# Optimization experiments

Hardware: AMD Instinct MI355X
Metric: run time of the kernel (lower is better)

The kernel has to match this reference:

```python
import jax, jax.numpy as jnp
import numpy as np

B, S = 1, 2048
HIDDEN = 2560
NH, NKV, HD = 32, 8, 128
GS = 128  # awq group size
ROPE_THETA = 1000000.0


def dequant_q4(qweight, scales, qzeros):
    """Unpack int4 AWQ weights -> dense [K, N] float weight.
    qweight: [K//8, N] int32, 8 nibbles packed along the input (K) dim.
    scales/qzeros: [K//GS, N]. w = (nibble - zero) * scale.
    """
    K8, N = qweight.shape
    shifts = jnp.arange(8, dtype=jnp.int32) * 4
    nib = (qweight[:, None, :] >> shifts[None, :, None]) & 0xF  # [K//8, 8, N]
    w = nib.reshape(K8 * 8, N).astype(scales.dtype)             # [K, N]
    z = jnp.repeat(qzeros.astype(scales.dtype), GS, axis=0)     # [K, N]
    s = jnp.repeat(scales, GS, axis=0)                          # [K, N]
    return (w - z) * s


def linear_q4(x, qw, sc, qz, bias=None):
    w = dequant_q4(qw, sc, qz)                     # [K, N]
    y = jnp.einsum('bsk,kn->bsn', x, w)
    return y + bias if bias is not None else y


def rotate_half(x):
    x1, x2 = jnp.split(x, 2, axis=-1)
    return jnp.concatenate([-x2, x1], axis=-1)


def apply_rope(q, k, cos, sin):
    # cos/sin: [B, S, HD] -> broadcast over heads at dim 2
    c = cos[:, :, None, :]
    s = sin[:, :, None, :]
    return q * c + rotate_half(q) * s, k * c + rotate_half(k) * s


def setup_inputs() -> dict:
    key = jax.random.key(0)
    ks = jax.random.split(key, 12)

    x = jax.random.normal(ks[0], (B, S, HIDDEN), dtype=jnp.float32)

    # genuine rotary embedding tables
    inv_freq = 1.0 / (ROPE_THETA ** (np.arange(0, HD, 2, dtype=np.float32) / HD))
    t = np.arange(S, dtype=np.float32)
    freqs = np.outer(t, inv_freq)                      # [S, HD/2]
    emb = np.concatenate([freqs, freqs], axis=-1)      # [S, HD]
    cos = jnp.asarray(np.cos(emb)[None], dtype=jnp.float32)  # [1, S, HD]
    sin = jnp.asarray(np.sin(emb)[None], dtype=jnp.float32)

    def mk_proj(kq, ksc, kz, K, N, group=GS):
        qw = jax.random.randint(kq, (K // 8, N), 0, 2**31 - 1, dtype=jnp.int32)
        sc = jax.random.normal(ksc, (K // group, N), dtype=jnp.float32) * 0.01
        qz = jax.random.randint(kz, (K // group, N), 0, 16, dtype=jnp.int32)
        return qw, sc, qz

    q_qweight, q_scales, q_qzeros = mk_proj(ks[1], ks[2], ks[3], HIDDEN, NH * HD)
    k_qweight, k_scales, k_qzeros = mk_proj(ks[4], ks[5], ks[6], HIDDEN, NKV * HD)
    v_qweight, v_scales, v_qzeros = mk_proj(ks[7], ks[8], ks[9], HIDDEN, NKV * HD)
    o_qweight, o_scales, o_qzeros = mk_proj(ks[10], ks[11], jax.random.fold_in(key, 99), NH * HD, HIDDEN)

    kb = jax.random.split(jax.random.fold_in(key, 7), 3)
    q_bias = jax.random.normal(kb[0], (NH * HD,), dtype=jnp.float32) * 0.02
    k_bias = jax.random.normal(kb[1], (NKV * HD,), dtype=jnp.float32) * 0.02
    v_bias = jax.random.normal(kb[2], (NKV * HD,), dtype=jnp.float32) * 0.02

    return dict(x=x, cos=cos, sin=sin,
                q_scales=q_scales, q_bias=q_bias,
                k_scales=k_scales, k_bias=k_bias,
                v_scales=v_scales, v_bias=v_bias,
                o_scales=o_scales,
                q_qweight=q_qweight, q_qzeros=q_qzeros,
                k_qweight=k_qweight, k_qzeros=k_qzeros,
                v_qweight=v_qweight, v_qzeros=v_qzeros,
                o_qweight=o_qweight, o_qzeros=o_qzeros)


def reference(x, cos, sin,
              q_scales, q_bias, k_scales, k_bias, v_scales, v_bias, o_scales,
              q_qweight, q_qzeros, k_qweight, k_qzeros,
              v_qweight, v_qzeros, o_qweight, o_qzeros):
    b, s, _ = x.shape
    xq = linear_q4(x, q_qweight, q_scales, q_qzeros, q_bias).reshape(b, s, NH, HD)
    xk = linear_q4(x, k_qweight, k_scales, k_qzeros, k_bias).reshape(b, s, NKV, HD)
    xv = linear_q4(x, v_qweight, v_scales, v_qzeros, v_bias).reshape(b, s, NKV, HD)

    xq, xk = apply_rope(xq, xk, cos, sin)

    # GQA: repeat KV heads to match query heads (prefill, start_pos=0)
    rep = NH // NKV
    xk = jnp.repeat(xk, rep, axis=2)   # [b, s, NH, HD]
    xv = jnp.repeat(xv, rep, axis=2)

    scale = 1.0 / jnp.sqrt(jnp.asarray(HD, dtype=xq.dtype))
    scores = jnp.einsum('bqhd,bkhd->bhqk', xq, xk) * scale  # [b, NH, s, s]
    causal = jnp.tril(jnp.ones((s, s), dtype=bool))
    scores = jnp.where(causal[None, None], scores, jnp.finfo(scores.dtype).min)
    attn = jax.nn.softmax(scores, axis=-1)
    out = jnp.einsum('bhqk,bkhd->bqhd', attn, xv).reshape(b, s, NH * HD)

    return linear_q4(out, o_qweight, o_scales, o_qzeros)  # [b, s, HIDDEN]
```

## Files before the change

### kernel.cpp

```cpp
#include <hip/hip_runtime.h>
#include <hip/hip_bf16.h>
#include <cstdint>

#define S_LEN 2048
#define HIDDEN 2560
#define NH 32
#define NKV 8
#define HD 128
#define GS 128

typedef __attribute__((ext_vector_type(8))) _Float16 half8v;
typedef __attribute__((ext_vector_type(2))) _Float16 half2v;
typedef __attribute__((ext_vector_type(4))) float f32x4;
typedef unsigned int uint;
typedef unsigned short ushort;

__device__ inline ushort f2h(float f) {
    _Float16 h = (_Float16)f;
    return __builtin_bit_cast(ushort, h);
}
__device__ inline float h2f(ushort u) {
    return (float)__builtin_bit_cast(_Float16, u);
}
__device__ inline uint pk2(ushort a, ushort b) { return (uint)a | ((uint)b << 16); }

__device__ __attribute__((always_inline)) inline void gl_lds16(const void* g, void* l) {
    __builtin_amdgcn_global_load_lds(
        (const __attribute__((address_space(1))) unsigned int*)g,
        (__attribute__((address_space(3))) unsigned int*)l, 16, 0, 0);
}

#define WAIT_LGKM0  asm volatile("s_waitcnt lgkmcnt(0)" ::: "memory")
#define WAIT_VM(N)  asm volatile("s_waitcnt vmcnt(" #N ")" ::: "memory")
#define RAW_BARRIER { __builtin_amdgcn_s_barrier(); __builtin_amdgcn_sched_barrier(0); }

__global__ __launch_bounds__(320) void xcvt_kernel(
    const float* __restrict__ X, ushort* __restrict__ Xf)
{
    const int row = blockIdx.x;
    const int t   = threadIdx.x;
    const size_t base = (size_t)row * HIDDEN + t * 8;
    float4 a = *(const float4*)&X[base];
    float4 b = *(const float4*)&X[base + 4];
    uint4 hw = {pk2(f2h(a.x), f2h(a.y)), pk2(f2h(a.z), f2h(a.w)),
                pk2(f2h(b.x), f2h(b.y)), pk2(f2h(b.z), f2h(b.w))};
    *(uint4*)&Xf[base] = hw;
}

__global__ __launch_bounds__(256) void qkv9_kernel(
    const ushort* __restrict__ Xf,
    const int* __restrict__ q_qw, const float* __restrict__ q_sc,
    const int* __restrict__ q_qz, const float* __restrict__ q_b,
    const int* __restrict__ k_qw, const float* __restrict__ k_sc,
    const int* __restrict__ k_qz, const float* __restrict__ k_b,
    const int* __restrict__ v_qw, const float* __restrict__ v_sc,
    const int* __restrict__ v_qz, const float* __restrict__ v_b,
    const float* __restrict__ cosb, const float* __restrict__ sinb,
    ushort* __restrict__ Qf, ushort* __restrict__ Kf,
    ushort* __restrict__ Vrm)
{
    __shared__ __align__(16) char LDSB[65536];
    ushort* A0 = (ushort*)(LDSB);
    ushort* A1 = (ushort*)(LDSB + 16384);
    ushort* B0 = (ushort*)(LDSB + 32768);
    ushort* B1 = (ushort*)(LDSB + 49152);

    const int t  = threadIdx.x;
    const int w  = t >> 6;
    const int l  = t & 63;
    const int lg = l >> 4;
    const int lr = l & 15;
    const int wr = w >> 1;
    const int wc = w & 1;
    const int K  = HIDDEN;

    const int bid = blockIdx.x;
    const int swz = (bid & 7) * 96 + (bid >> 3);
    const int nblk = swz % 48;
    const int m0   = (swz / 48) * 128;

    int region, nbase, Nw;
    const int* QW; const float* SC; const int* QZ; const float* BI;
    if (nblk < 32)      { region = 0; nbase = nblk * 128;        Nw = NH * HD;
                          QW = q_qw; SC = q_sc; QZ = q_qz; BI = q_b; }
    else if (nblk < 40) { region = 1; nbase = (nblk - 32) * 128; Nw = NKV * HD;
                          QW = k_qw; SC = k_sc; QZ = k_qz; BI = k_b; }
    else                { region = 2; nbase = (nblk - 40) * 128; Nw = NKV * HD;
                          QW = v_qw; SC = v_sc; QZ = v_qz; BI = v_b; }

    const int ldsAw = w * 1024;
    size_t aoff[4];
#pragma unroll
    for (int i = 0; i < 4; ++i) {
        int slot = i * 256 + t;
        int am = slot >> 3, ac = slot & 7;
        aoff[i] = (size_t)(m0 + am) * K + (size_t)((ac ^ (am & 7)) * 8);
    }
    const int bn  = t & 127;
    const int bk0 = (t >> 7) * 4;
    int bwoff[4];
#pragma unroll
    for (int j = 0; j < 4; ++j)
        bwoff[j] = (bn * 128 + (bk0 + j) * 16) ^ ((bn & 7) << 4);

    int ncm[4];
#pragma unroll
    for (int nf = 0; nf < 4; ++nf)
        ncm[nf] = wc * 32 + (nf & 1) * 16 + lr + ((nf & 2) ? 64 : 0);

    const int xorA = (lr & 7) << 4;
    int aroff[4][2], broff[4][2];
#pragma unroll
    for (int mf = 0; mf < 4; ++mf)
#pragma unroll
        for (int ks = 0; ks < 2; ++ks)
            aroff[mf][ks] = (((wr * 64 + mf * 16 + lr) * 128) + lg * 16 + ks * 64) ^ xorA;
#pragma unroll
    for (int nf = 0; nf < 4; ++nf)
#pragma unroll
        for (int ks = 0; ks < 2; ++ks)
            broff[nf][ks] = ((ncm[nf] * 128) + lg * 16 + ks * 64) ^ xorA;

    f32x4 macc[4][4];
#pragma unroll
    for (int mf = 0; mf < 4; ++mf)
#pragma unroll
        for (int nf = 0; nf < 4; ++nf) macc[mf][nf] = f32x4{0.f, 0.f, 0.f, 0.f};
    uint qr[4];
    float scf, zf;

#define QKV_QW(tile) { int g8 = (tile) * 8; int gg = (tile) >> 1; \
    _Pragma("unroll") \
    for (int j = 0; j < 4; ++j) \
        qr[j] = (uint)QW[(size_t)(g8 + bk0 + j) * Nw + nbase + bn]; \
    scf = SC[(size_t)gg * Nw + nbase + bn]; \
    zf  = (float)QZ[(size_t)gg * Nw + nbase + bn]; }

#define QKV_STAGE_A(AH, k0) { \
    gl_lds16(Xf + (k0) + aoff[0], (char*)(AH) + ldsAw); \
    gl_lds16(Xf + (k0) + aoff[1], (char*)(AH) + 4096 + ldsAw); \
    gl_lds16(Xf + (k0) + aoff[2], (char*)(AH) + 8192 + ldsAw); \
    gl_lds16(Xf + (k0) + aoff[3], (char*)(AH) + 12288 + ldsAw); }

#define QKV_BWRITE(BT) { \
    ushort sch = f2h(scf); \
    float schf = h2f(sch); \
    ushort msc = f2h(-128.0f * schf);    \
    ushort nzs = f2h(-(zf * schf)); \
    half2v S2 = {__builtin_bit_cast(_Float16, sch), __builtin_bit_cast(_Float16, sch)}; \
    half2v M2 = {__builtin_bit_cast(_Float16, msc), __builtin_bit_cast(_Float16, msc)}; \
    half2v Z2 = {__builtin_bit_cast(_Float16, nzs), __builtin_bit_cast(_Float16, nzs)}; \
    _Pragma("unroll") \
    for (int j = 0; j < 4; ++j) { \
        uint q = qr[j]; \
        uint xn = q & 0x0F0F0F0Fu; \
        uint yn = (q >> 4) & 0x0F0F0F0Fu; \
        uint4 dw; \
        uint W0 = __builtin_amdgcn_perm(yn, xn, 0x0C040C00u); \
        uint W1 = __builtin_amdgcn_perm(yn, xn, 0x0C050C01u); \
        uint W2 = __builtin_amdgcn_perm(yn, xn, 0x0C060C02u); \
        uint W3 = __builtin_amdgcn_perm(yn, xn, 0x0C070C03u); \
        uint e0 = (W0 << 3) | 0x58005800u; \
        uint e1 = (W1 << 3) | 0x58005800u; \
        uint e2 = (W2 << 3) | 0x58005800u; \
        uint e3 = (W3 << 3) | 0x58005800u; \
        half2v w0 = __builtin_bit_cast(half2v, e0) * S2 + M2; w0 = w0 + Z2; \
        half2v w1 = __builtin_bit_cast(half2v, e1) * S2 + M2; w1 = w1 + Z2; \
        half2v w2 = __builtin_bit_cast(half2v, e2) * S2 + M2; w2 = w2 + Z2; \
        half2v w3 = __builtin_bit_cast(half2v, e3) * S2 + M2; w3 = w3 + Z2; \
        dw.x = __builtin_bit_cast(uint, w0); \
        dw.y = __builtin_bit_cast(uint, w1); \
        dw.z = __builtin_bit_cast(uint, w2); \
        dw.w = __builtin_bit_cast(uint, w3); \
        *(uint4*)((char*)(BT) + bwoff[j]) = dw; \
    } }

#define QKV_COMPUTE(AH, BT) { \
    _Pragma("unroll") \
    for (int ks = 0; ks < 2; ++ks) { \
        half8v av[4], bv[4]; \
        _Pragma("unroll") \
        for (int mf = 0; mf < 4; ++mf) \
            av[mf] = *(const half8v*)((const char*)(AH) + aroff[mf][ks]); \
        _Pragma("unroll") \
        for (int nf = 0; nf < 4; ++nf) \
            bv[nf] = *(const half8v*)((const char*)(BT) + broff[nf][ks]); \
        _Pragma("unroll") \
        for (int mf = 0; mf < 4; ++mf) \
            _Pragma("unroll") \
            for (int nf = 0; nf < 4; ++nf) \
                macc[mf][nf] = __builtin_amdgcn_mfma_f32_16x16x32_f16(av[mf], bv[nf], macc[mf][nf], 0, 0, 0); \
    } }

    QKV_QW(0);
    QKV_BWRITE(B0);
    QKV_STAGE_A(A0, 0);
    QKV_QW(1);
    WAIT_LGKM0;
    WAIT_VM(6);
    RAW_BARRIER;

    for (int g = 0; g < 19; ++g) {
        QKV_STAGE_A(A1, (2 * g + 1) * 64);
        QKV_COMPUTE(A0, B0);
        QKV_BWRITE(B1);
        QKV_QW(2 * g + 2);
        WAIT_LGKM0;
        WAIT_VM(6);
        RAW_BARRIER;
        QKV_STAGE_A(A0, (2 * g + 2) * 64);
        QKV_COMPUTE(A1, B1);
        QKV_BWRITE(B0);
        QKV_QW(2 * g + 3);
        WAIT_LGKM0;
        WAIT_VM(6);
        RAW_BARRIER;
    }
    QKV_STAGE_A(A1, 39 * 64);
    QKV_COMPUTE(A0, B0);
    QKV_BWRITE(B1);
    WAIT_LGKM0;
    WAIT_VM(0);
    RAW_BARRIER;
    QKV_COMPUTE(A1, B1);

#pragma unroll
    for (int nf = 0; nf < 4; ++nf) {
        float bv = BI[nbase + ncm[nf]];
#pragma unroll
        for (int mf = 0; mf < 4; ++mf)
#pragma unroll
            for (int r = 0; r < 4; ++r) macc[mf][nf][r] += bv;
    }

    if (region == 2) {
#pragma unroll
        for (int mf = 0; mf < 4; ++mf)
#pragma unroll
            for (int r = 0; r < 4; ++r) {
                int row = m0 + wr * 64 + mf * 16 + lg * 4 + r;
#pragma unroll
                for (int nf = 0; nf < 4; ++nf)
                    Vrm[(size_t)row * (NKV * HD) + nbase + ncm[nf]] = f2h(macc[mf][nf][r]);
            }
    } else {
        ushort* OF = (region == 0) ? Qf : Kf;
        const int No = (region == 0) ? NH * HD : NKV * HD;
        const float osc = (region == 0) ? 0.08838834764831845f : 1.0f;
#pragma unroll
        for (int mf = 0; mf < 4; ++mf)
#pragma unroll
            for (int r = 0; r < 4; ++r) {
                int row = m0 + wr * 64 + mf * 16 + lg * 4 + r;
                const float* cb = &cosb[(size_t)row * HD];
                const float* sb = &sinb[(size_t)row * HD];
#pragma unroll
                for (int nf = 0; nf < 2; ++nf) {
                    int d = wc * 32 + nf * 16 + lr;
                    float a = macc[mf][nf][r];
                    float b = macc[mf][nf + 2][r];
                    float o1 = (a * cb[d]      - b * sb[d])      * osc;
                    float o2 = (b * cb[d + 64] + a * sb[d + 64]) * osc;
                    OF[(size_t)row * No + nbase + d]      = f2h(o1);
                    OF[(size_t)row * No + nbase + d + 64] = f2h(o2);
                }
            }
    }
#undef QKV_QW
#undef QKV_STAGE_A
#undef QKV_BWRITE
#undef QKV_COMPUTE
}

__global__ __launch_bounds__(256) void vtrans_kernel(
    const ushort* __restrict__ Vrm, ushort* __restrict__ VfT)
{
    __shared__ ushort Ts[64][65];
    const int s0 = blockIdx.x * 64;
    const int n0 = blockIdx.y * 64;
    const int t  = threadIdx.x;
    {
        int r = t >> 2, c0 = (t & 3) * 16;
        uint4 v0 = *(const uint4*)&Vrm[(size_t)(s0 + r) * (NKV * HD) + n0 + c0];
        uint4 v1 = *(const uint4*)&Vrm[(size_t)(s0 + r) * (NKV * HD) + n0 + c0 + 8];
        const ushort* pv = (const ushort*)&v0;
#pragma unroll
        for (int j = 0; j < 8; ++j) Ts[r][c0 + j] = pv[j];
        pv = (const ushort*)&v1;
#pragma unroll
        for (int j = 0; j < 8; ++j) Ts[r][c0 + 8 + j] = pv[j];
    }
    __syncthreads();
    {
        int rn = t >> 2, cs0 = (t & 3) * 16;
        ushort ob[16];
#pragma unroll
        for (int j = 0; j < 16; ++j) ob[j] = Ts[cs0 + j][rn];
        ushort* dst = &VfT[(size_t)(n0 + rn) * S_LEN + s0 + cs0];
        *(uint4*)dst = ((uint4*)ob)[0];
        *(uint4*)(dst + 8) = ((uint4*)ob)[1];
    }
}

__global__ __launch_bounds__(256) void oproj8_kernel(
    const ushort* __restrict__ Xb, const int* __restrict__ QW,
    const float* __restrict__ SC, const int* __restrict__ QZ,
    float* __restrict__ Y)
{
    __shared__ __align__(16) char LDSB[65536];
    ushort* A0 = (ushort*)(LDSB);
    ushort* A1 = (ushort*)(LDSB + 16384);
    ushort* B0 = (ushort*)(LDSB + 32768);
    ushort* B1 = (ushort*)(LDSB + 49152);

    const int t  = threadIdx.x;
    const int w  = t >> 6;
    const int l  = t & 63;
    const int lg = l >> 4;
    const int lr = l & 15;
    const int wr = w >> 1;
    const int wc = w & 1;
    const int K  = NH * HD;
    const int N  = HIDDEN;

    const int bid = blockIdx.x;
    const int swz = (bid & 7) * 40 + (bid >> 3);
    const int n0  = (swz % 20) * 128;
    const int m0  = (swz / 20) * 128;

    const int ldsAw = w * 1024;
    size_t aoff[4];
#pragma unroll
    for (int i = 0; i < 4; ++i) {
        int slot = i * 256 + t;
        int am = slot >> 3, ac = slot & 7;
        aoff[i] = (size_t)(m0 + am) * K + (size_t)((ac ^ (am & 7)) * 8);
    }
    const int bn  = t & 127;
    const int bk0 = (t >> 7) * 4;
    int bwoff[4];
#pragma unroll
    for (int j = 0; j < 4; ++j)
        bwoff[j] = (bn * 128 + (bk0 + j) * 16) ^ ((bn & 7) << 4);

    const int xorA = (lr & 7) << 4;
    int aroff[4][2], broff[4][2];
#pragma unroll
    for (int mf = 0; mf < 4; ++mf)
#pragma unroll
        for (int ks = 0; ks < 2; ++ks)
            aroff[mf][ks] = (((wr * 64 + mf * 16 + lr) * 128) + lg * 16 + ks * 64) ^ xorA;
#pragma unroll
    for (int nf = 0; nf < 4; ++nf)
#pragma unroll
        for (int ks = 0; ks < 2; ++ks)
            broff[nf][ks] = (((wc * 64 + nf * 16 + lr) * 128) + lg * 16 + ks * 64) ^ xorA;

    f32x4 macc[4][4];
#pragma unroll
    for (int mf = 0; mf < 4; ++mf)
#pragma unroll
        for (int nf = 0; nf < 4; ++nf) macc[mf][nf] = f32x4{0.f, 0.f, 0.f, 0.f};
    uint qr[4];
    float scf, zf;

#define OP_QW(tile) { int g8 = (tile) * 8; int gg = (tile) >> 1; \
    _Pragma("unroll") \
    for (int j = 0; j < 4; ++j) \
        qr[j] = (uint)QW[(size_t)(g8 + bk0 + j) * N + n0 + bn]; \
    scf = SC[(size_t)gg * N + n0 + bn]; \
    zf  = (float)QZ[(size_t)gg * N + n0 + bn]; }

#define OP_STAGE_A(AH, k0) { \
    gl_lds16(Xb + (k0) + aoff[0], (char*)(AH) + ldsAw); \
    gl_lds16(Xb + (k0) + aoff[1], (char*)(AH) + 4096 + ldsAw); \
    gl_lds16(Xb + (k0) + aoff[2], (char*)(AH) + 8192 + ldsAw); \
    gl_lds16(Xb + (k0) + aoff[3], (char*)(AH) + 12288 + ldsAw); }

#define OP_BWRITE(BT) { \
    ushort sch = f2h(scf); \
    float schf = h2f(sch); \
    ushort msc = f2h(-128.0f * schf); \
    ushort nzs = f2h(-(zf * schf)); \
    half2v S2 = {__builtin_bit_cast(_Float16, sch), __builtin_bit_cast(_Float16, sch)}; \
    half2v M2 = {__builtin_bit_cast(_Float16, msc), __builtin_bit_cast(_Float16, msc)}; \
    half2v Z2 = {__builtin_bit_cast(_Float16, nzs), __builtin_bit_cast(_Float16, nzs)}; \
    _Pragma("unroll") \
    for (int j = 0; j < 4; ++j) { \
        uint q = qr[j]; \
        uint xn = q & 0x0F0F0F0Fu; \
        uint yn = (q >> 4) & 0x0F0F0F0Fu; \
        uint4 dw; \
        uint W0 = __builtin_amdgcn_perm(yn, xn, 0x0C040C00u); \
        uint W1 = __builtin_amdgcn_perm(yn, xn, 0x0C050C01u); \
        uint W2 = __builtin_amdgcn_perm(yn, xn, 0x0C060C02u); \
        uint W3 = __builtin_amdgcn_perm(yn, xn, 0x0C070C03u); \
        uint e0 = (W0 << 3) | 0x58005800u; \
        uint e1 = (W1 << 3) | 0x58005800u; \
        uint e2 = (W2 << 3) | 0x58005800u; \
        uint e3 = (W3 << 3) | 0x58005800u; \
        half2v w0 = __builtin_bit_cast(half2v, e0) * S2 + M2; w0 = w0 + Z2; \
        half2v w1 = __builtin_bit_cast(half2v, e1) * S2 + M2; w1 = w1 + Z2; \
        half2v w2 = __builtin_bit_cast(half2v, e2) * S2 + M2; w2 = w2 + Z2; \
        half2v w3 = __builtin_bit_cast(half2v, e3) * S2 + M2; w3 = w3 + Z2; \
        dw.x = __builtin_bit_cast(uint, w0); \
        dw.y = __builtin_bit_cast(uint, w1); \
        dw.z = __builtin_bit_cast(uint, w2); \
        dw.w = __builtin_bit_cast(uint, w3); \
        *(uint4*)((char*)(BT) + bwoff[j]) = dw; \
    } }

#define OP_COMPUTE(AH, BT) { \
    _Pragma("unroll") \
    for (int ks = 0; ks < 2; ++ks) { \
        half8v av[4], bv[4]; \
        _Pragma("unroll") \
        for (int mf = 0; mf < 4; ++mf) \
            av[mf] = *(const half8v*)((const char*)(AH) + aroff[mf][ks]); \
        _Pragma("unroll") \
        for (int nf = 0; nf < 4; ++nf) \
            bv[nf] = *(const half8v*)((const char*)(BT) + broff[nf][ks]); \
        _Pragma("unroll") \
        for (int mf = 0; mf < 4; ++mf) \
            _Pragma("unroll") \
            for (int nf = 0; nf < 4; ++nf) \
                macc[mf][nf] = __builtin_amdgcn_mfma_f32_16x16x32_f16(av[mf], bv[nf], macc[mf][nf], 0, 0, 0); \
    } }

    OP_QW(0);
    OP_BWRITE(B0);
    OP_STAGE_A(A0, 0);
    OP_QW(1);
    WAIT_LGKM0;
    WAIT_VM(6);
    RAW_BARRIER;

    for (int g = 0; g < 31; ++g) {
        OP_STAGE_A(A1, (2 * g + 1) * 64);
        OP_COMPUTE(A0, B0);
        OP_BWRITE(B1);
        OP_QW(2 * g + 2);
        WAIT_LGKM0;
        WAIT_VM(6);
        RAW_BARRIER;
        OP_STAGE_A(A0, (2 * g + 2) * 64);
        OP_COMPUTE(A1, B1);
        OP_BWRITE(B0);
        OP_QW(2 * g + 3);
        WAIT_LGKM0;
        WAIT_VM(6);
        RAW_BARRIER;
    }
    OP_STAGE_A(A1, 63 * 64);
    OP_COMPUTE(A0, B0);
    OP_BWRITE(B1);
    WAIT_LGKM0;
    WAIT_VM(0);
    RAW_BARRIER;
    OP_COMPUTE(A1, B1);

#pragma unroll
    for (int mf = 0; mf < 4; ++mf)
#pragma unroll
        for (int r = 0; r < 4; ++r) {
            int row = m0 + wr * 64 + mf * 16 + lg * 4 + r;
#pragma unroll
            for (int nf = 0; nf < 4; ++nf)
                Y[(size_t)row * N + n0 + wc * 64 + nf * 16 + lr] = macc[mf][nf][r];
        }
#undef OP_QW
#undef OP_STAGE_A
#undef OP_BWRITE
#undef OP_COMPUTE
}

__global__ __launch_bounds__(256) void attn_mfma_kernel(
    const ushort* __restrict__ Qh,
    const ushort* __restrict__ Kh,
    const ushort* __restrict__ Vt,
    ushort* __restrict__ AO)
{
    __shared__ ushort Ks0[32 * 128];
    __shared__ ushort Ks1[32 * 128];
    __shared__ ushort Vs0[128 * 32];
    __shared__ ushort Vs1[128 * 32];
    __shared__ __align__(16) char PsB[4 * 1280];

    const int h  = blockIdx.x;
    const int qb = gridDim.y - 1 - blockIdx.y;
    const int s0 = qb * 64;
    const int t  = threadIdx.x;
    const int w  = t >> 6;
    const int l  = t & 63;
    const int lg = l >> 4;
    const int lr = l & 15;
    const int kvh = h >> 2;
    const int qw = s0 + w * 16;
    const int q  = qw + lr;

    half8v qf[4];
#pragma unroll
    for (int d = 0; d < 4; ++d) {
        size_t off = (size_t)q * (NH * HD) + h * HD + d * 32 + lg * 8;
        qf[d] = *(const half8v*)&Qh[off];
    }

    f32x4 o[8];
#pragma unroll
    for (int i = 0; i < 8; ++i) o[i] = f32x4{0.f, 0.f, 0.f, 0.f};
    float m = -1e30f, lsum = 0.f;
    char* pw = PsB + w * 1280;

#define ATTN_STAGE(KB, VB, k0) { \
    _Pragma("unroll") \
    for (int i = 0; i < 2; ++i) { \
        int slot = w * 128 + i * 64 + l; \
        int mr = slot >> 4, c = slot & 15; \
        size_t goff = (size_t)((k0) + mr) * (NKV * HD) + kvh * HD + ((c ^ (mr & 7)) * 8); \
        gl_lds16(Kh + goff, (char*)(KB) + (w * 128 + i * 64) * 16); \
    } \
    _Pragma("unroll") \
    for (int i = 0; i < 2; ++i) { \
        int slot = w * 128 + i * 64 + l; \
        int dim = slot >> 2, c = slot & 3; \
        size_t goff = (size_t)(kvh * HD + dim) * S_LEN + (k0) + ((c ^ (dim & 3)) * 8); \
        gl_lds16(Vt + goff, (char*)(VB) + (w * 128 + i * 64) * 16); \
    } }

#define ATTN_TILE(KSF, VSS, k0) \
    if ((k0) <= qw + 15) { \
        f32x4 s_[2]; \
        s_[0] = f32x4{0.f, 0.f, 0.f, 0.f}; \
        s_[1] = f32x4{0.f, 0.f, 0.f, 0.f}; \
        _Pragma("unroll") \
        for (int d = 0; d < 4; ++d) { \
            _Pragma("unroll") \
            for (int nt2 = 0; nt2 < 2; ++nt2) { \
                int row = nt2 * 16 + lr; \
                int off = row * 256 + ((d * 64 + lg * 16) ^ ((row & 7) << 4)); \
                half8v kf = *(const half8v*)((const char*)(KSF) + off); \
                s_[nt2] = __builtin_amdgcn_mfma_f32_16x16x32_f16(kf, qf[d], s_[nt2], 0, 0, 0); \
            } \
        } \
        float sv[8]; \
        _Pragma("unroll") \
        for (int nt2 = 0; nt2 < 2; ++nt2) \
            _Pragma("unroll") \
            for (int r = 0; r < 4; ++r) { \
                int kv = (k0) + nt2 * 16 + lg * 4 + r; \
                sv[nt2 * 4 + r] = (kv <= q) ? s_[nt2][r] : -1e30f; \
            } \
        float mx = sv[0]; \
        _Pragma("unroll") \
        for (int j = 1; j < 8; ++j) mx = fmaxf(mx, sv[j]); \
        mx = fmaxf(mx, __shfl_xor(mx, 16)); \
        mx = fmaxf(mx, __shfl_xor(mx, 32)); \
        float mnew = fmaxf(m, mx); \
        float resc = __expf(m - mnew); \
        m = mnew; \
        float p_[8], ps = 0.f; \
        _Pragma("unroll") \
        for (int j = 0; j < 8; ++j) { p_[j] = __expf(sv[j] - mnew); ps += p_[j]; } \
        ps += __shfl_xor(ps, 16); \
        ps += __shfl_xor(ps, 32); \
        lsum = lsum * resc + ps; \
        _Pragma("unroll") \
        for (int dt = 0; dt < 8; ++dt) \
            _Pragma("unroll") \
            for (int r = 0; r < 4; ++r) o[dt][r] *= resc; \
        uint2 w0_ = {pk2(f2h(p_[0]), f2h(p_[1])), pk2(f2h(p_[2]), f2h(p_[3]))}; \
        uint2 w1_ = {pk2(f2h(p_[4]), f2h(p_[5])), pk2(f2h(p_[6]), f2h(p_[7]))}; \
        *(uint2*)(pw + lr * 80 + lg * 8)      = w0_; \
        *(uint2*)(pw + lr * 80 + 32 + lg * 8) = w1_; \
        asm volatile("s_waitcnt lgkmcnt(0)" ::: "memory"); \
        half8v pf = *(const half8v*)(pw + lr * 80 + lg * 16); \
        _Pragma("unroll") \
        for (int dt = 0; dt < 8; ++dt) { \
            int dim = dt * 16 + lr; \
            half8v vf = *(const half8v*)((const char*)(VSS) + dim * 64 + ((lg * 16) ^ ((dim & 3) << 4))); \
            o[dt] = __builtin_amdgcn_mfma_f32_16x16x32_f16(vf, pf, o[dt], 0, 0, 0); \
        } \
    }

    const int ntiles = qb * 2 + 2;

    ATTN_STAGE(Ks0, Vs0, 0);
    WAIT_VM(0);
    RAW_BARRIER;

    for (int kt = 0; kt < ntiles; kt += 2) {
        if (kt + 1 < ntiles) ATTN_STAGE(Ks1, Vs1, (kt + 1) * 32);
        ATTN_TILE(Ks0, Vs0, kt * 32);
        WAIT_VM(0);
        RAW_BARRIER;
        if (kt + 2 < ntiles) ATTN_STAGE(Ks0, Vs0, (kt + 2) * 32);
        ATTN_TILE(Ks1, Vs1, (kt + 1) * 32);
        WAIT_VM(0);
        RAW_BARRIER;
    }

    float inv = 1.f / lsum;
    ushort* dst = &AO[(size_t)q * (NH * HD) + h * HD];
#pragma unroll
    for (int dt = 0; dt < 8; ++dt) {
        uint2 ov = {pk2(f2h(o[dt][0] * inv), f2h(o[dt][1] * inv)),
                    pk2(f2h(o[dt][2] * inv), f2h(o[dt][3] * inv))};
        *(uint2*)(dst + dt * 16 + lg * 4) = ov;
    }
#undef ATTN_STAGE
#undef ATTN_TILE
}

extern "C" void kernel_launch(void* const* d_in, const int* in_sizes, int n_in,
                              void* d_out, int out_size, void* d_ws, size_t ws_size,
                              hipStream_t stream)
{
    const float* x    = (const float*)d_in[0];
    const float* cosb = (const float*)d_in[1];
    const float* sinb = (const float*)d_in[2];
    const float* q_sc = (const float*)d_in[3];
    const float* q_b  = (const float*)d_in[4];
    const float* k_sc = (const float*)d_in[5];
    const float* k_b  = (const float*)d_in[6];
    const float* v_sc = (const float*)d_in[7];
    const float* v_b  = (const float*)d_in[8];
    const float* o_sc = (const float*)d_in[9];
    const int* q_qw   = (const int*)d_in[10];
    const int* q_qz   = (const int*)d_in[11];
    const int* k_qw   = (const int*)d_in[12];
    const int* k_qz   = (const int*)d_in[13];
    const int* v_qw   = (const int*)d_in[14];
    const int* v_qz   = (const int*)d_in[15];
    const int* o_qw   = (const int*)d_in[16];
    const int* o_qz   = (const int*)d_in[17];
    float* out = (float*)d_out;

    char* ws = (char*)d_ws;
    ushort* Xf   = (ushort*)ws;
    ushort* AOf  = (ushort*)ws;
    ushort* Qf   = (ushort*)(ws + (size_t)16 * 1024 * 1024);
    ushort* Kf   = (ushort*)(ws + (size_t)32 * 1024 * 1024);
    ushort* Vrm  = (ushort*)(ws + (size_t)36 * 1024 * 1024);
    ushort* VfT  = (ushort*)(ws + (size_t)40 * 1024 * 1024);

    xcvt_kernel<<<S_LEN, 320, 0, stream>>>(x, Xf);

    qkv9_kernel<<<768, 256, 0, stream>>>(
        Xf,
        q_qw, q_sc, q_qz, q_b,
        k_qw, k_sc, k_qz, k_b,
        v_qw, v_sc, v_qz, v_b,
        cosb, sinb, Qf, Kf, Vrm);

    vtrans_kernel<<<dim3(S_LEN / 64, (NKV * HD) / 64), 256, 0, stream>>>(Vrm, VfT);

    attn_mfma_kernel<<<dim3(NH, S_LEN / 64), 256, 0, stream>>>(Qf, Kf, VfT, AOf);

    oproj8_kernel<<<320, 256, 0, stream>>>(
        AOf, o_qw, o_sc, o_qz, out);
}
```

Measured before the change: 259.9 us.

## Split QKV weight dequant into separate pre-pass kernel feeding plain fp16 GEMM

Moves the int4 AWQ dequantization out of the QKV GEMM main loop into a dedicated kernel that writes a transposed fp16 weight matrix WT to workspace once. The GEMM then streams both X and WT tiles via direct global-to-LDS loads, with no in-loop unpacking. Each 128-column weight tile was previously dequantized once for every one of the 16 row-blocks, so this removes that redundant ALU work. The cost is an extra launch and roughly 15 MB of fp16 weight traffic. The wait is now vmcnt(0) each stage, which weakens prefetch overlap.

```diff
diff --git a/kernel.cpp b/kernel.cpp
--- a/kernel.cpp
+++ b/kernel.cpp
@@ -47,14 +47,75 @@
     *(uint4*)&Xf[base] = hw;
 }
 
-__global__ __launch_bounds__(256) void qkv9_kernel(
-    const ushort* __restrict__ Xf,
-    const int* __restrict__ q_qw, const float* __restrict__ q_sc,
-    const int* __restrict__ q_qz, const float* __restrict__ q_b,
-    const int* __restrict__ k_qw, const float* __restrict__ k_sc,
-    const int* __restrict__ k_qz, const float* __restrict__ k_b,
-    const int* __restrict__ v_qw, const float* __restrict__ v_sc,
-    const int* __restrict__ v_qz, const float* __restrict__ v_b,
+__global__ __launch_bounds__(256) void wdq_kernel(
+    const int* __restrict__ q_qw, const float* __restrict__ q_sc, const int* __restrict__ q_qz,
+    const int* __restrict__ k_qw, const float* __restrict__ k_sc, const int* __restrict__ k_qz,
+    const int* __restrict__ v_qw, const float* __restrict__ v_sc, const int* __restrict__ v_qz,
+    ushort* __restrict__ WT)
+{
+    __shared__ __align__(16) char Ts[16384];
+
+    const int bx = blockIdx.x;
+    const int kt = blockIdx.y;
+    const int t  = threadIdx.x;
+
+    int nloc0, wtbase, Nw;
+    const int* QW; const float* SC; const int* QZ;
+    if (bx < 64)      { Nw = NH * HD;  nloc0 = bx * 64;        wtbase = bx * 64;
+                        QW = q_qw; SC = q_sc; QZ = q_qz; }
+    else if (bx < 80) { Nw = NKV * HD; nloc0 = (bx - 64) * 64; wtbase = 4096 + nloc0;
+                        QW = k_qw; SC = k_sc; QZ = k_qz; }
+    else              { Nw = NKV * HD; nloc0 = (bx - 80) * 64; wtbase = 5120 + nloc0;
+                        QW = v_qw; SC = v_sc; QZ = v_qz; }
+
+    const int k80 = kt * 16;
+    const int nn  = t & 63;
+    const float scf = SC[(size_t)kt * Nw + nloc0 + nn];
+    const float zf  = (float)QZ[(size_t)kt * Nw + nloc0 + nn];
+    ushort sch = f2h(scf);
+    float schf = h2f(sch);
+    ushort msc = f2h(-128.0f * schf);
+    ushort nzs = f2h(-(zf * schf));
+    half2v S2 = {__builtin_bit_cast(_Float16, sch), __builtin_bit_cast(_Float16, sch)};
+    half2v M2 = {__builtin_bit_cast(_Float16, msc), __builtin_bit_cast(_Float16, msc)};
+    half2v Z2 = {__builtin_bit_cast(_Float16, nzs), __builtin_bit_cast(_Float16, nzs)};
+
+#pragma unroll
+    for (int i = 0; i < 4; ++i) {
+        int kw = i * 4 + (t >> 6);
+        uint q = (uint)QW[(size_t)(k80 + kw) * Nw + nloc0 + nn];
+        uint xn = q & 0x0F0F0F0Fu;
+        uint yn = (q >> 4) & 0x0F0F0F0Fu;
+        uint W0 = __builtin_amdgcn_perm(yn, xn, 0x0C040C00u);
+        uint W1 = __builtin_amdgcn_perm(yn, xn, 0x0C050C01u);
+        uint W2 = __builtin_amdgcn_perm(yn, xn, 0x0C060C02u);
+        uint W3 = __builtin_amdgcn_perm(yn, xn, 0x0C070C03u);
+        uint e0 = (W0 << 3) | 0x58005800u;
+        uint e1 = (W1 << 3) | 0x58005800u;
+        uint e2 = (W2 << 3) | 0x58005800u;
+        uint e3 = (W3 << 3) | 0x58005800u;
+        half2v w0 = __builtin_bit_cast(half2v, e0) * S2 + M2; w0 = w0 + Z2;
+        half2v w1 = __builtin_bit_cast(half2v, e1) * S2 + M2; w1 = w1 + Z2;
+        half2v w2 = __builtin_bit_cast(half2v, e2) * S2 + M2; w2 = w2 + Z2;
+        half2v w3 = __builtin_bit_cast(half2v, e3) * S2 + M2; w3 = w3 + Z2;
+        uint4 dw = {__builtin_bit_cast(uint, w0), __builtin_bit_cast(uint, w1),
+                    __builtin_bit_cast(uint, w2), __builtin_bit_cast(uint, w3)};
+        *(uint4*)(Ts + nn * 256 + ((kw * 16) ^ ((nn & 7) << 4))) = dw;
+    }
+    __syncthreads();
+    const int kc = t & 15;
+#pragma unroll
+    for (int i = 0; i < 4; ++i) {
+        int nr = i * 16 + (t >> 4);
+        uint4 v = *(const uint4*)(Ts + nr * 256 + ((kc * 16) ^ ((nr & 7) << 4)));
+        *(uint4*)&WT[(size_t)(wtbase + nr) * HIDDEN + kt * 128 + kc * 8] = v;
+    }
+}
+
+__global__ __launch_bounds__(256) void qkv10_kernel(
+    const ushort* __restrict__ Xf, const ushort* __restrict__ WT,
+    const float* __restrict__ q_b, const float* __restrict__ k_b,
+    const float* __restrict__ v_b,
     const float* __restrict__ cosb, const float* __restrict__ sinb,
     ushort* __restrict__ Qf, ushort* __restrict__ Kf,
     ushort* __restrict__ Vrm)
@@ -78,30 +139,23 @@
     const int swz = (bid & 7) * 96 + (bid >> 3);
     const int nblk = swz % 48;
     const int m0   = (swz / 48) * 128;
-
-    int region, nbase, Nw;
-    const int* QW; const float* SC; const int* QZ; const float* BI;
-    if (nblk < 32)      { region = 0; nbase = nblk * 128;        Nw = NH * HD;
-                          QW = q_qw; SC = q_sc; QZ = q_qz; BI = q_b; }
-    else if (nblk < 40) { region = 1; nbase = (nblk - 32) * 128; Nw = NKV * HD;
-                          QW = k_qw; SC = k_sc; QZ = k_qz; BI = k_b; }
-    else                { region = 2; nbase = (nblk - 40) * 128; Nw = NKV * HD;
-                          QW = v_qw; SC = v_sc; QZ = v_qz; BI = v_b; }
+    const int wtrow = nblk * 128;
+
+    int region, nbase;
+    const float* BI;
+    if (nblk < 32)      { region = 0; nbase = nblk * 128;        BI = q_b; }
+    else if (nblk < 40) { region = 1; nbase = (nblk - 32) * 128; BI = k_b; }
+    else                { region = 2; nbase = (nblk - 40) * 128; BI = v_b; }
 
     const int ldsAw = w * 1024;
-    size_t aoff[4];
+    size_t aoff[4], boff[4];
 #pragma unroll
     for (int i = 0; i < 4; ++i) {
         int slot = i * 256 + t;
-        int am = slot >> 3, ac = slot & 7;
-        aoff[i] = (size_t)(m0 + am) * K + (size_t)((ac ^ (am & 7)) * 8);
-    }
-    const int bn  = t & 127;
-    const int bk0 = (t >> 7) * 4;
-    int bwoff[4];
-#pragma unroll
-    for (int j = 0; j < 4; ++j)
-        bwoff[j] = (bn * 128 + (bk0 + j) * 16) ^ ((bn & 7) << 4);
+        int rm = slot >> 3, rc = slot & 7;
+        aoff[i] = (size_t)(m0 + rm) * K + (size_t)((rc ^ (rm & 7)) * 8);
+        boff[i] = (size_t)(wtrow + rm) * K + (size_t)((rc ^ (rm & 7)) * 8);
+    }
 
     int ncm[4];
 #pragma unroll
@@ -126,54 +180,16 @@
     for (int mf = 0; mf < 4; ++mf)
 #pragma unroll
         for (int nf = 0; nf < 4; ++nf) macc[mf][nf] = f32x4{0.f, 0.f, 0.f, 0.f};
-    uint qr[4];
-    float scf, zf;
-
-#define QKV_QW(tile) { int g8 = (tile) * 8; int gg = (tile) >> 1; \
-    _Pragma("unroll") \
-    for (int j = 0; j < 4; ++j) \
-        qr[j] = (uint)QW[(size_t)(g8 + bk0 + j) * Nw + nbase + bn]; \
-    scf = SC[(size_t)gg * Nw + nbase + bn]; \
-    zf  = (float)QZ[(size_t)gg * Nw + nbase + bn]; }
-
-#define QKV_STAGE_A(AH, k0) { \
+
+#define QKV_STAGE(AH, BH, k0) { \
     gl_lds16(Xf + (k0) + aoff[0], (char*)(AH) + ldsAw); \
     gl_lds16(Xf + (k0) + aoff[1], (char*)(AH) + 4096 + ldsAw); \
     gl_lds16(Xf + (k0) + aoff[2], (char*)(AH) + 8192 + ldsAw); \
-    gl_lds16(Xf + (k0) + aoff[3], (char*)(AH) + 12288 + ldsAw); }
-
-#define QKV_BWRITE(BT) { \
-    ushort sch = f2h(scf); \
-    float schf = h2f(sch); \
-    ushort msc = f2h(-128.0f * schf);    \
-    ushort nzs = f2h(-(zf * schf)); \
-    half2v S2 = {__builtin_bit_cast(_Float16, sch), __builtin_bit_cast(_Float16, sch)}; \
-    half2v M2 = {__builtin_bit_cast(_Float16, msc), __builtin_bit_cast(_Float16, msc)}; \
-    half2v Z2 = {__builtin_bit_cast(_Float16, nzs), __builtin_bit_cast(_Float16, nzs)}; \
-    _Pragma("unroll") \
-    for (int j = 0; j < 4; ++j) { \
-        uint q = qr[j]; \
-        uint xn = q & 0x0F0F0F0Fu; \
-        uint yn = (q >> 4) & 0x0F0F0F0Fu; \
-        uint4 dw; \
-        uint W0 = __builtin_amdgcn_perm(yn, xn, 0x0C040C00u); \
-        uint W1 = __builtin_amdgcn_perm(yn, xn, 0x0C050C01u); \
-        uint W2 = __builtin_amdgcn_perm(yn, xn, 0x0C060C02u); \
-        uint W3 = __builtin_amdgcn_perm(yn, xn, 0x0C070C03u); \
-        uint e0 = (W0 << 3) | 0x58005800u; \
-        uint e1 = (W1 << 3) | 0x58005800u; \
-        uint e2 = (W2 << 3) | 0x58005800u; \
-        uint e3 = (W3 << 3) | 0x58005800u; \
-        half2v w0 = __builtin_bit_cast(half2v, e0) * S2 + M2; w0 = w0 + Z2; \
-        half2v w1 = __builtin_bit_cast(half2v, e1) * S2 + M2; w1 = w1 + Z2; \
-        half2v w2 = __builtin_bit_cast(half2v, e2) * S2 + M2; w2 = w2 + Z2; \
-        half2v w3 = __builtin_bit_cast(half2v, e3) * S2 + M2; w3 = w3 + Z2; \
-        dw.x = __builtin_bit_cast(uint, w0); \
-        dw.y = __builtin_bit_cast(uint, w1); \
-        dw.z = __builtin_bit_cast(uint, w2); \
-        dw.w = __builtin_bit_cast(uint, w3); \
-        *(uint4*)((char*)(BT) + bwoff[j]) = dw; \
-    } }
+    gl_lds16(Xf + (k0) + aoff[3], (char*)(AH) + 12288 + ldsAw); \
+    gl_lds16(WT + (k0) + boff[0], (char*)(BH) + ldsAw); \
+    gl_lds16(WT + (k0) + boff[1], (char*)(BH) + 4096 + ldsAw); \
+    gl_lds16(WT + (k0) + boff[2], (char*)(BH) + 8192 + ldsAw); \
+    gl_lds16(WT + (k0) + boff[3], (char*)(BH) + 12288 + ldsAw); }
 
 #define QKV_COMPUTE(AH, BT) { \
     _Pragma("unroll") \
@@ -192,34 +208,22 @@
                 macc[mf][nf] = __builtin_amdgcn_mfma_f32_16x16x32_f16(av[mf], bv[nf], macc[mf][nf], 0, 0, 0); \
     } }
 
-    QKV_QW(0);
-    QKV_BWRITE(B0);
-    QKV_STAGE_A(A0, 0);
-    QKV_QW(1);
-    WAIT_LGKM0;
-    WAIT_VM(6);
+    QKV_STAGE(A0, B0, 0);
+    WAIT_VM(0);
     RAW_BARRIER;
 
     for (int g = 0; g < 19; ++g) {
-        QKV_STAGE_A(A1, (2 * g + 1) * 64);
+        QKV_STAGE(A1, B1, (2 * g + 1) * 64);
         QKV_COMPUTE(A0, B0);
-        QKV_BWRITE(B1);
-        QKV_QW(2 * g + 2);
-        WAIT_LGKM0;
-        WAIT_VM(6);
+        WAIT_VM(0);
         RAW_BARRIER;
-        QKV_STAGE_A(A0, (2 * g + 2) * 64);
+        QKV_STAGE(A0, B0, (2 * g + 2) * 64);
         QKV_COMPUTE(A1, B1);
-        QKV_BWRITE(B0);
-        QKV_QW(2 * g + 3);
-        WAIT_LGKM0;
-        WAIT_VM(6);
+        WAIT_VM(0);
         RAW_BARRIER;
     }
-    QKV_STAGE_A(A1, 39 * 64);
+    QKV_STAGE(A1, B1, 39 * 64);
     QKV_COMPUTE(A0, B0);
-    QKV_BWRITE(B1);
-    WAIT_LGKM0;
     WAIT_VM(0);
     RAW_BARRIER;
     QKV_COMPUTE(A1, B1);
@@ -266,9 +270,7 @@
                 }
             }
     }
-#undef QKV_QW
-#undef QKV_STAGE_A
-#undef QKV_BWRITE
+#undef QKV_STAGE
 #undef QKV_COMPUTE
 }
 
@@ -638,19 +640,19 @@
     char* ws = (char*)d_ws;
     ushort* Xf   = (ushort*)ws;
     ushort* AOf  = (ushort*)ws;
-    ushort* Qf   = (ushort*)(ws + (size_t)16 * 1024 * 1024);
-    ushort* Kf   = (ushort*)(ws + (size_t)32 * 1024 * 1024);
-    ushort* Vrm  = (ushort*)(ws + (size_t)36 * 1024 * 1024);
-    ushort* VfT  = (ushort*)(ws + (size_t)40 * 1024 * 1024);
+    ushort* WT   = (ushort*)(ws + (size_t)10 * 1024 * 1024);
+    ushort* Qf   = (ushort*)(ws + (size_t)40 * 1024 * 1024);
+    ushort* Kf   = (ushort*)(ws + (size_t)56 * 1024 * 1024);
+    ushort* Vrm  = (ushort*)(ws + (size_t)60 * 1024 * 1024);
+    ushort* VfT  = (ushort*)(ws + (size_t)64 * 1024 * 1024);
 
     xcvt_kernel<<<S_LEN, 320, 0, stream>>>(x, Xf);
 
-    qkv9_kernel<<<768, 256, 0, stream>>>(
-        Xf,
-        q_qw, q_sc, q_qz, q_b,
-        k_qw, k_sc, k_qz, k_b,
-        v_qw, v_sc, v_qz, v_b,
-        cosb, sinb, Qf, Kf, Vrm);
+    wdq_kernel<<<dim3(96, 20), 256, 0, stream>>>(
+        q_qw, q_sc, q_qz, k_qw, k_sc, k_qz, v_qw, v_sc, v_qz, WT);
+
+    qkv10_kernel<<<768, 256, 0, stream>>>(
+        Xf, WT, q_b, k_b, v_b, cosb, sinb, Qf, Kf, Vrm);
 
     vtrans_kernel<<<dim3(S_LEN / 64, (NKV * HD) / 64), 256, 0, stream>>>(Vrm, VfT);
 
```

After: 269.8 us. 3.8% more time.
